# Performance work log

Measured on AMD Instinct MI355X. Metric: run time of the kernel, lower is better.

Reference implementation:

```python
import jax, jax.numpy as jnp
import numpy as np

SCALE = 0.08838834764831845  # 1/sqrt(128)
NUM_HEADS = 32
NUM_KV_HEADS = 8
HEAD_DIM = 128
BLOCK_SIZE = 16
NUM_BLOCKS = 4096
MAX_BLOCKS_PER_SEQ = 128
BATCH = 32
MAX_CTX = MAX_BLOCKS_PER_SEQ * BLOCK_SIZE  # 2048


def setup_inputs() -> dict:
    key = jax.random.key(0)
    ks = jax.random.split(key, 8)
    D = NUM_KV_HEADS * HEAD_DIM
    q = jax.random.normal(ks[0], (BATCH, NUM_HEADS, HEAD_DIM), dtype=jnp.float32)
    k = jax.random.normal(ks[1], (BATCH, NUM_KV_HEADS, HEAD_DIM), dtype=jnp.float32)
    v = jax.random.normal(ks[2], (BATCH, NUM_KV_HEADS, HEAD_DIM), dtype=jnp.float32)
    k_cache = jax.random.normal(ks[3], (NUM_BLOCKS, BLOCK_SIZE, D), dtype=jnp.float32)
    v_cache = jax.random.normal(ks[4], (NUM_BLOCKS, BLOCK_SIZE, D), dtype=jnp.float32)
    # one unique slot per decoding request (deterministic scatter)
    slot_mapping = jnp.arange(BATCH, dtype=jnp.int32)
    block_tables = jax.random.randint(ks[5], (BATCH, MAX_BLOCKS_PER_SEQ), 0, NUM_BLOCKS, dtype=jnp.int32)
    context_lens = jnp.maximum(
        jax.random.randint(ks[6], (BATCH,), 0, MAX_CTX, dtype=jnp.int32), 1)
    return {"q": q, "k": k, "v": v, "k_cache": k_cache, "v_cache": v_cache,
            "slot_mapping": slot_mapping, "block_tables": block_tables,
            "context_lens": context_lens}


def reference(q, k, v, k_cache, v_cache, slot_mapping, block_tables, context_lens):
    B, H, Dh = q.shape
    KVH = k.shape[1]
    num_blocks, block_size, D = k_cache.shape
    n_rep = H // KVH

    # --- store_kvcache: scatter new K/V tokens into the paged cache ---
    # flat slot index = block_idx * block_size + slot_idx; slot == -1 dropped
    kc = k_cache.reshape(num_blocks * block_size, D)
    vc = v_cache.reshape(num_blocks * block_size, D)
    kc = kc.at[slot_mapping].set(k.reshape(B, D), mode="drop")
    vc = vc.at[slot_mapping].set(v.reshape(B, D), mode="drop")
    kc = kc.reshape(num_blocks, block_size, D)
    vc = vc.reshape(num_blocks, block_size, D)

    # --- decode-phase paged attention ---
    # gather per-request KV via block tables: [B, S, KVH, Dh]
    k_seq = kc[block_tables].reshape(B, -1, KVH, Dh)
    v_seq = vc[block_tables].reshape(B, -1, KVH, Dh)
    S = k_seq.shape[1]

    # GQA: group query heads over kv heads
    qg = q.reshape(B, KVH, n_rep, Dh)
    scores = jnp.einsum("bkgd,bskd->bkgs", qg, k_seq) * SCALE  # [B,KVH,G,S]
    valid = jnp.arange(S, dtype=jnp.int32)[None, :] < context_lens[:, None]  # [B,S]
    scores = jnp.where(valid[:, None, None, :], scores, jnp.float32(-1e30))
    p = jax.nn.softmax(scores, axis=-1)
    out = jnp.einsum("bkgs,bskd->bkgd", p, v_seq)
    return out.reshape(B, H, Dh)
```

## Files before the change

### kernel.cpp

```cpp
#include <hip/hip_runtime.h>
#include <math.h>

#define NH      32
#define KVH     8
#define GRP     4
#define DH      128
#define BS      16
#define D_TOT   1024
#define MBPS    128
#define SPLIT_TOK 256
#define NSPLIT  8
#define SCALE_F 0.08838834764831845f

__global__ void store_kv_kernel(const float* __restrict__ k,
                                const float* __restrict__ v,
                                float* __restrict__ kc,
                                float* __restrict__ vc,
                                const int* __restrict__ slot_mapping) {
    int b = blockIdx.x;
    int t = threadIdx.x;
    int s = slot_mapping[b];
    if (s < 0) return;
    const float4* k4 = (const float4*)(k + (size_t)b * D_TOT);
    const float4* v4 = (const float4*)(v + (size_t)b * D_TOT);
    float4* kc4 = (float4*)(kc + (size_t)s * D_TOT);
    float4* vc4 = (float4*)(vc + (size_t)s * D_TOT);
    kc4[t] = k4[t];
    vc4[t] = v4[t];
}

__global__ __launch_bounds__(256) void attn_partial_kernel(
    const float* __restrict__ q,
    const float* __restrict__ kc,
    const float* __restrict__ vc,
    const int* __restrict__ block_tables,
    const int* __restrict__ ctx_lens,
    float* __restrict__ ws)
{
    const int kvh   = blockIdx.x;
    const int b     = blockIdx.y;
    const int split = blockIdx.z;
    const int ctx   = ctx_lens[b];
    const int start = split * SPLIT_TOK;
    if (start >= ctx) return;
    const int end = min(ctx, start + SPLIT_TOK);

    const int wave = threadIdx.x >> 6;
    const int lane = threadIdx.x & 63;
    const int h    = kvh * GRP + wave;
    const int dseg = lane & 15;
    const int tsub = lane >> 4;

    const float* qh = q + ((size_t)b * NH + h) * DH;
    const float4 q0 = *(const float4*)(qh + dseg * 4);
    const float4 q1 = *(const float4*)(qh + 64 + dseg * 4);

    const int* bt = block_tables + b * MBPS;

    float  m = -INFINITY;
    float  l = 0.f;
    float2 acc = make_float2(0.f, 0.f);

    for (int t0 = start; t0 < end; t0 += 4) {
        int tok  = t0 + tsub;
        int tokc = min(tok, end - 1);
        int blk  = bt[tokc >> 4];
        const float* krow = kc + ((size_t)blk * BS + (tokc & 15)) * D_TOT + kvh * DH;
        float4 k0 = *(const float4*)(krow + dseg * 4);
        float4 k1 = *(const float4*)(krow + 64 + dseg * 4);
        float p = q0.x*k0.x + q0.y*k0.y + q0.z*k0.z + q0.w*k0.w
                + q1.x*k1.x + q1.y*k1.y + q1.z*k1.z + q1.w*k1.w;
        p += __shfl_xor(p, 1);
        p += __shfl_xor(p, 2);
        p += __shfl_xor(p, 4);
        p += __shfl_xor(p, 8);
        float s = p * SCALE_F;
        if (tok >= end) s = -INFINITY;

        float s0 = __shfl(s, 0);
        float s1 = __shfl(s, 16);
        float s2 = __shfl(s, 32);
        float s3 = __shfl(s, 48);

        float mnew = fmaxf(fmaxf(fmaxf(fmaxf(m, s0), s1), s2), s3);
        float alpha = __expf(m - mnew);
        float p0 = __expf(s0 - mnew);
        float p1 = __expf(s1 - mnew);
        float p2 = __expf(s2 - mnew);
        float p3 = __expf(s3 - mnew);
        l = l * alpha + (p0 + p1 + p2 + p3);
        acc.x *= alpha;
        acc.y *= alpha;

        #pragma unroll
        for (int j = 0; j < 4; ++j) {
            int tc = min(t0 + j, end - 1);
            int blkj = bt[tc >> 4];
            const float* vrow = vc + ((size_t)blkj * BS + (tc & 15)) * D_TOT + kvh * DH;
            float2 vv = *(const float2*)(vrow + 2 * lane);
            float pj = (j == 0) ? p0 : (j == 1) ? p1 : (j == 2) ? p2 : p3;
            acc.x += pj * vv.x;
            acc.y += pj * vv.y;
        }
        m = mnew;
    }

    float* o = ws + ((((size_t)b * KVH + kvh) * NSPLIT + split) * GRP + wave) * 130;
    *(float2*)(o + 2 * lane) = acc;
    if (lane == 0) { o[128] = m; o[129] = l; }
}

__global__ void combine_kernel(const float* __restrict__ ws,
                               const int* __restrict__ ctx_lens,
                               float* __restrict__ out)
{
    int bh = blockIdx.x;
    int b  = bh >> 5;
    int h  = bh & 31;
    int kvh = h >> 2;
    int g   = h & 3;
    int d   = threadIdx.x;
    int ctx = ctx_lens[b];
    int nsp = (ctx + SPLIT_TOK - 1) / SPLIT_TOK;

    const float* base = ws + ((size_t)b * KVH + kvh) * NSPLIT * GRP * 130 + (size_t)g * 130;
    const int stride = GRP * 130;

    float M = -INFINITY;
    for (int i = 0; i < nsp; ++i)
        M = fmaxf(M, base[i * stride + 128]);

    float L = 0.f, O = 0.f;
    for (int i = 0; i < nsp; ++i) {
        const float* p = base + i * stride;
        float w = __expf(p[128] - M);
        L += p[129] * w;
        O += p[d] * w;
    }
    out[((size_t)b * NH + h) * DH + d] = O / L;
}

extern "C" void kernel_launch(void* const* d_in, const int* in_sizes, int n_in,
                              void* d_out, int out_size, void* d_ws, size_t ws_size,
                              hipStream_t stream) {
    const float* q  = (const float*)d_in[0];
    const float* k  = (const float*)d_in[1];
    const float* v  = (const float*)d_in[2];
    float* kc       = (float*)d_in[3];
    float* vc       = (float*)d_in[4];
    const int* slot = (const int*)d_in[5];
    const int* bt   = (const int*)d_in[6];
    const int* cl   = (const int*)d_in[7];
    float* out      = (float*)d_out;
    float* ws       = (float*)d_ws;

    store_kv_kernel<<<32, 256, 0, stream>>>(k, v, kc, vc, slot);
    attn_partial_kernel<<<dim3(KVH, 32, NSPLIT), 256, 0, stream>>>(q, kc, vc, bt, cl, ws);
    combine_kernel<<<1024, 128, 0, stream>>>(ws, cl, out);
}
```

Before: 545.7 us.

## Restructure paged attention loop per cache block with 8-wide lanes and more splits

The partial kernel now walks one cache block at a time, reading the block-table entry once per block. Each lane loads contiguous 8-float K and V segments, so the V loads become float4 and are shared with the token layout of the K loads instead of being reloaded per token. The online softmax rescales only when the running max grows, and the partial accumulators are reduced across token sub-groups at the end. The split count is chosen from the workspace size, up to 16, to give the GPU more blocks. The trade-off is a larger per-thread accumulator and a deferred cross-lane reduction.

```diff
diff --git a/kernel.cpp b/kernel.cpp
--- a/kernel.cpp
+++ b/kernel.cpp
@@ -8,9 +8,9 @@
 #define BS      16
 #define D_TOT   1024
 #define MBPS    128
-#define SPLIT_TOK 256
-#define NSPLIT  8
+#define MAX_CTX 2048
 #define SCALE_F 0.08838834764831845f
+#define PSTRIDE 136
 
 __global__ void store_kv_kernel(const float* __restrict__ k,
                                 const float* __restrict__ v,
@@ -29,90 +29,109 @@
     vc4[t] = v4[t];
 }
 
-__global__ __launch_bounds__(256) void attn_partial_kernel(
+__global__ __launch_bounds__(256, 6) void attn_partial_kernel(
     const float* __restrict__ q,
     const float* __restrict__ kc,
     const float* __restrict__ vc,
     const int* __restrict__ block_tables,
     const int* __restrict__ ctx_lens,
-    float* __restrict__ ws)
+    float* __restrict__ ws,
+    int split_tok, int nsplit)
 {
     const int kvh   = blockIdx.x;
     const int b     = blockIdx.y;
     const int split = blockIdx.z;
     const int ctx   = ctx_lens[b];
-    const int start = split * SPLIT_TOK;
+    const int start = split * split_tok;
     if (start >= ctx) return;
-    const int end = min(ctx, start + SPLIT_TOK);
+    const int end = min(ctx, start + split_tok);
 
     const int wave = threadIdx.x >> 6;
     const int lane = threadIdx.x & 63;
     const int h    = kvh * GRP + wave;
+    const int tsub = lane >> 4;
     const int dseg = lane & 15;
-    const int tsub = lane >> 4;
 
     const float* qh = q + ((size_t)b * NH + h) * DH;
-    const float4 q0 = *(const float4*)(qh + dseg * 4);
-    const float4 q1 = *(const float4*)(qh + 64 + dseg * 4);
+    const float4 qa = *(const float4*)(qh + dseg * 8);
+    const float4 qb = *(const float4*)(qh + dseg * 8 + 4);
 
     const int* bt = block_tables + b * MBPS;
 
-    float  m = -INFINITY;
-    float  l = 0.f;
-    float2 acc = make_float2(0.f, 0.f);
+    float m = -INFINITY;
+    float l = 0.f;
+    float acc[8];
+    #pragma unroll
+    for (int j = 0; j < 8; ++j) acc[j] = 0.f;
 
-    for (int t0 = start; t0 < end; t0 += 4) {
-        int tok  = t0 + tsub;
-        int tokc = min(tok, end - 1);
-        int blk  = bt[tokc >> 4];
-        const float* krow = kc + ((size_t)blk * BS + (tokc & 15)) * D_TOT + kvh * DH;
-        float4 k0 = *(const float4*)(krow + dseg * 4);
-        float4 k1 = *(const float4*)(krow + 64 + dseg * 4);
-        float p = q0.x*k0.x + q0.y*k0.y + q0.z*k0.z + q0.w*k0.w
-                + q1.x*k1.x + q1.y*k1.y + q1.z*k1.z + q1.w*k1.w;
-        p += __shfl_xor(p, 1);
-        p += __shfl_xor(p, 2);
-        p += __shfl_xor(p, 4);
-        p += __shfl_xor(p, 8);
-        float s = p * SCALE_F;
-        if (tok >= end) s = -INFINITY;
+    const int cb0 = start >> 4;
+    const int cb1 = (end + 15) >> 4;
 
-        float s0 = __shfl(s, 0);
-        float s1 = __shfl(s, 16);
-        float s2 = __shfl(s, 32);
-        float s3 = __shfl(s, 48);
+    for (int cb = cb0; cb < cb1; ++cb) {
+        const int blk = bt[cb];
+        const float* kbase = kc + (size_t)blk * BS * D_TOT + kvh * DH;
+        const float* vbase = vc + (size_t)blk * BS * D_TOT + kvh * DH;
+        const int tbase = cb << 4;
 
-        float mnew = fmaxf(fmaxf(fmaxf(fmaxf(m, s0), s1), s2), s3);
-        float alpha = __expf(m - mnew);
-        float p0 = __expf(s0 - mnew);
-        float p1 = __expf(s1 - mnew);
-        float p2 = __expf(s2 - mnew);
-        float p3 = __expf(s3 - mnew);
-        l = l * alpha + (p0 + p1 + p2 + p3);
-        acc.x *= alpha;
-        acc.y *= alpha;
+        #pragma unroll 2
+        for (int ps = 0; ps < 4; ++ps) {
+            const int tok  = tbase + ps * 4 + tsub;
+            const int rofs = (ps * 4 + tsub) * D_TOT + dseg * 8;
+            float4 ka = *(const float4*)(kbase + rofs);
+            float4 kb = *(const float4*)(kbase + rofs + 4);
+            float4 va = *(const float4*)(vbase + rofs);
+            float4 vb = *(const float4*)(vbase + rofs + 4);
 
-        #pragma unroll
-        for (int j = 0; j < 4; ++j) {
-            int tc = min(t0 + j, end - 1);
-            int blkj = bt[tc >> 4];
-            const float* vrow = vc + ((size_t)blkj * BS + (tc & 15)) * D_TOT + kvh * DH;
-            float2 vv = *(const float2*)(vrow + 2 * lane);
-            float pj = (j == 0) ? p0 : (j == 1) ? p1 : (j == 2) ? p2 : p3;
-            acc.x += pj * vv.x;
-            acc.y += pj * vv.y;
+            float s = qa.x*ka.x + qa.y*ka.y + qa.z*ka.z + qa.w*ka.w
+                    + qb.x*kb.x + qb.y*kb.y + qb.z*kb.z + qb.w*kb.w;
+            s += __shfl_xor(s, 1);
+            s += __shfl_xor(s, 2);
+            s += __shfl_xor(s, 4);
+            s += __shfl_xor(s, 8);
+            s *= SCALE_F;
+            if (tok >= end) s = -INFINITY;
+
+            float pm = fmaxf(s, __shfl_xor(s, 16));
+            pm = fmaxf(pm, __shfl_xor(pm, 32));
+
+            if (pm > m) {
+                float alpha = __expf(m - pm);
+                l *= alpha;
+                #pragma unroll
+                for (int j = 0; j < 8; ++j) acc[j] *= alpha;
+                m = pm;
+            }
+
+            float p = __expf(s - m);
+            float psum = p + __shfl_xor(p, 16);
+            psum += __shfl_xor(psum, 32);
+            l += psum;
+
+            acc[0] += p * va.x; acc[1] += p * va.y;
+            acc[2] += p * va.z; acc[3] += p * va.w;
+            acc[4] += p * vb.x; acc[5] += p * vb.y;
+            acc[6] += p * vb.z; acc[7] += p * vb.w;
         }
-        m = mnew;
     }
 
-    float* o = ws + ((((size_t)b * KVH + kvh) * NSPLIT + split) * GRP + wave) * 130;
-    *(float2*)(o + 2 * lane) = acc;
-    if (lane == 0) { o[128] = m; o[129] = l; }
+    #pragma unroll
+    for (int j = 0; j < 8; ++j) {
+        acc[j] += __shfl_xor(acc[j], 16);
+        acc[j] += __shfl_xor(acc[j], 32);
+    }
+
+    float* o = ws + ((((size_t)b * KVH + kvh) * nsplit + split) * GRP + wave) * PSTRIDE;
+    if (tsub == 0) {
+        *(float4*)(o + dseg * 8)     = make_float4(acc[0], acc[1], acc[2], acc[3]);
+        *(float4*)(o + dseg * 8 + 4) = make_float4(acc[4], acc[5], acc[6], acc[7]);
+        if (lane == 0) { o[128] = m; o[129] = l; }
+    }
 }
 
 __global__ void combine_kernel(const float* __restrict__ ws,
                                const int* __restrict__ ctx_lens,
-                               float* __restrict__ out)
+                               float* __restrict__ out,
+                               int split_tok, int nsplit)
 {
     int bh = blockIdx.x;
     int b  = bh >> 5;
@@ -121,10 +140,11 @@
     int g   = h & 3;
     int d   = threadIdx.x;
     int ctx = ctx_lens[b];
-    int nsp = (ctx + SPLIT_TOK - 1) / SPLIT_TOK;
+    int nsp = (ctx + split_tok - 1) / split_tok;
 
-    const float* base = ws + ((size_t)b * KVH + kvh) * NSPLIT * GRP * 130 + (size_t)g * 130;
-    const int stride = GRP * 130;
+    const float* base = ws + (((size_t)b * KVH + kvh) * nsplit + 0) * GRP * PSTRIDE
+                           + (size_t)g * PSTRIDE;
+    const int stride = GRP * PSTRIDE;
 
     float M = -INFINITY;
     for (int i = 0; i < nsp; ++i)
@@ -154,7 +174,15 @@
     float* out      = (float*)d_out;
     float* ws       = (float*)d_ws;
 
+    const size_t per_split = (size_t)32 * KVH * GRP * PSTRIDE * sizeof(float);
+    int nsplit;
+    if      (ws_size >= per_split * 16) nsplit = 16;
+    else if (ws_size >= per_split * 8)  nsplit = 8;
+    else                                nsplit = 4;
+    int split_tok = MAX_CTX / nsplit;
+
     store_kv_kernel<<<32, 256, 0, stream>>>(k, v, kc, vc, slot);
-    attn_partial_kernel<<<dim3(KVH, 32, NSPLIT), 256, 0, stream>>>(q, kc, vc, bt, cl, ws);
-    combine_kernel<<<1024, 128, 0, stream>>>(ws, cl, out);
+    attn_partial_kernel<<<dim3(KVH, 32, nsplit), 256, 0, stream>>>(
+        q, kc, vc, bt, cl, ws, split_tok, nsplit);
+    combine_kernel<<<1024, 128, 0, stream>>>(ws, cl, out, split_tok, nsplit);
 }
```

New measurement: 491.0 us. -10.0%, faster.
